# Kernel tuning notes

Hardware: AMD Instinct MI355X
Metric: run time of the kernel (lower is better)

Reference implementation:

```python
import jax, jax.numpy as jnp
import numpy as np
import math

D_MODEL = 1024
NUM_HEADS = 16
HEAD_DIM = D_MODEL // NUM_HEADS
BLOCK_SIZE = 64
THRESHOLD = 0.99


def setup_inputs() -> dict:
    key = jax.random.key(0)
    ks = jax.random.split(key, 12)
    B, S, D = 2, 2048, D_MODEL
    scale = 1.0 / math.sqrt(D)
    x = jax.random.normal(ks[0], (B, S, D), dtype=jnp.float32)
    G_ii = jax.random.uniform(ks[1], (B, S), dtype=jnp.float32)
    # Linear weights stored as [in, out]; applied as x @ W + b (matches nn.Linear math).
    Wq = jax.random.normal(ks[2], (D, D), dtype=jnp.float32) * scale
    bq = jnp.zeros((D,), dtype=jnp.float32)
    Wk = jax.random.normal(ks[3], (D, D), dtype=jnp.float32) * scale
    bk = jnp.zeros((D,), dtype=jnp.float32)
    Wv = jax.random.normal(ks[4], (D, D), dtype=jnp.float32) * scale
    bv = jnp.zeros((D,), dtype=jnp.float32)
    Wo = jax.random.normal(ks[5], (D, D), dtype=jnp.float32) * scale
    bo = jnp.zeros((D,), dtype=jnp.float32)
    return {"x": x, "G_ii": G_ii, "Wq": Wq, "bq": bq, "Wk": Wk, "bk": bk,
            "Wv": Wv, "bv": bv, "Wo": Wo, "bo": bo}


def reference(x, G_ii, Wq, bq, Wk, bk, Wv, bv, Wo, bo):
    B, S, D = x.shape
    H, hd, bs = NUM_HEADS, HEAD_DIM, BLOCK_SIZE
    nb = S // bs

    # Projections and head split: [B, H, S, hd]
    q = (x @ Wq + bq).reshape(B, S, H, hd).transpose(0, 2, 1, 3)
    k = (x @ Wk + bk).reshape(B, S, H, hd).transpose(0, 2, 1, 3)
    v = (x @ Wv + bv).reshape(B, S, H, hd).transpose(0, 2, 1, 3)

    # Per-query-block scattering energy keep mask: block kept iff max |G_ii| >= threshold
    energy = jnp.abs(G_ii)                              # [B, S]
    block_max = energy.reshape(B, nb, bs).max(axis=-1)  # [B, nb]
    keep = (block_max >= THRESHOLD)                     # [B, nb] bool
    row_keep = jnp.repeat(keep, bs, axis=1)             # [B, S]

    # Kept query blocks attend densely (non-causal) over all keys; skipped blocks output zero.
    scores = jnp.einsum('bhqd,bhkd->bhqk', q, k) / math.sqrt(hd)  # [B, H, S, S]
    attn = jax.nn.softmax(scores, axis=-1)
    out = jnp.einsum('bhqk,bhkd->bhqd', attn, v)                  # [B, H, S, hd]
    out = out * row_keep[:, None, :, None].astype(out.dtype)

    out = out.transpose(0, 2, 1, 3).reshape(B, S, D)
    return out @ Wo + bo
```

## Files before the change

kernel.cpp:

```cpp
#include <hip/hip_runtime.h>
#include <math.h>

#define D_MODEL   1024
#define NUM_HEADS 16
#define HEAD_DIM  64
#define BS        64
#define NB        32
#define S_LEN     2048
#define BATCH     2
#define M_ROWS    (BATCH * S_LEN)
#define THRESH    0.99f
#define SCEXP     0.18033688f
#define NPH       (BATCH * NB * NUM_HEADS)

typedef __attribute__((ext_vector_type(8))) short bf16x8;
typedef __attribute__((ext_vector_type(8))) _Float16 f16x8;
typedef __attribute__((ext_vector_type(2))) __fp16 fp16v2;
typedef __attribute__((ext_vector_type(4))) float f32x4;

static constexpr size_t QKV_ELEMS = (size_t)BATCH * NUM_HEADS * S_LEN * HEAD_DIM;

__device__ __forceinline__ unsigned short f2bf(float f) {
    unsigned int u = __float_as_uint(f);
    u += 0x7fff + ((u >> 16) & 1);
    return (unsigned short)(u >> 16);
}

__device__ __forceinline__ unsigned int pkrtz(float a, float b) {
    fp16v2 r = __builtin_amdgcn_cvt_pkrtz(a, b);
    return __builtin_bit_cast(unsigned int, r);
}

__device__ __forceinline__ void gload16(const void* gptr, void* lptr) {
    __builtin_amdgcn_global_load_lds(
        (const __attribute__((address_space(1))) void*)gptr,
        (__attribute__((address_space(3))) void*)lptr, 16, 0, 0);
}

__global__ void compact_kernel(const float* __restrict__ G, int* __restrict__ keep,
                               int* __restrict__ work) {
    int t = threadIdx.x;
    const float4* g = (const float4*)(G + (size_t)t * 64);
    float mx = 0.f;
    #pragma unroll
    for (int i = 0; i < 16; i++) {
        float4 v = g[i];
        mx = fmaxf(mx, fmaxf(fmaxf(fabsf(v.x), fabsf(v.y)), fmaxf(fabsf(v.z), fabsf(v.w))));
    }
    bool k = (mx >= THRESH);
    unsigned long long bal = __ballot(k);
    int nk = __popcll(bal);
    unsigned long long below = bal & ((1ull << t) - 1ull);
    int nbelow = (int)__popcll(below);
    keep[t] = k ? 1 : 0;
    if (t == 0) work[0] = nk;
    int pos = k ? nbelow : (nk + t - nbelow);
    work[1 + pos] = t;
}

__global__ __launch_bounds__(256) void convert_x(const float* __restrict__ x,
                                                 unsigned short* __restrict__ xb) {
    size_t i = ((size_t)blockIdx.x * 256 + threadIdx.x) * 8;
    float4 a = *(const float4*)(x + i);
    float4 b = *(const float4*)(x + i + 4);
    uint4 o;
    o.x = (unsigned int)f2bf(a.x) | ((unsigned int)f2bf(a.y) << 16);
    o.y = (unsigned int)f2bf(a.z) | ((unsigned int)f2bf(a.w) << 16);
    o.z = (unsigned int)f2bf(b.x) | ((unsigned int)f2bf(b.y) << 16);
    o.w = (unsigned int)f2bf(b.z) | ((unsigned int)f2bf(b.w) << 16);
    *(uint4*)(xb + i) = o;
}

__global__ __launch_bounds__(256) void transpose_w(
    const float* __restrict__ Wq, const float* __restrict__ Wk,
    const float* __restrict__ Wv, const float* __restrict__ Wo,
    unsigned short* __restrict__ wcat, unsigned short* __restrict__ wot)
{
    int mat = blockIdx.z;
    const float* W = (mat == 0) ? Wq : (mat == 1) ? Wk : (mat == 2) ? Wv : Wo;
    __shared__ float T[64][65];
    int k0 = blockIdx.x * 64, n0 = blockIdx.y * 64;
    int tid = threadIdx.x;
    int rr = tid >> 4, c4 = (tid & 15) * 4;
    #pragma unroll
    for (int i = 0; i < 4; i++) {
        int row = rr + i * 16;
        float4 v = *(const float4*)(W + (size_t)(k0 + row) * 1024 + n0 + c4);
        T[row][c4 + 0] = v.x; T[row][c4 + 1] = v.y;
        T[row][c4 + 2] = v.z; T[row][c4 + 3] = v.w;
    }
    __syncthreads();
    unsigned short* dst = (mat < 3) ? (wcat + (size_t)mat * 1024 * 1024) : wot;
    #pragma unroll
    for (int i = 0; i < 4; i++) {
        int n = rr + i * 16;
        unsigned int lo = (unsigned int)f2bf(T[c4 + 0][n]) | ((unsigned int)f2bf(T[c4 + 1][n]) << 16);
        unsigned int hi = (unsigned int)f2bf(T[c4 + 2][n]) | ((unsigned int)f2bf(T[c4 + 3][n]) << 16);
        *(uint2*)(dst + (size_t)(n0 + n) * 1024 + k0 + c4) = make_uint2(lo, hi);
    }
}

__global__ __launch_bounds__(256) void mfma_gemm(
    const unsigned short* __restrict__ A, const unsigned short* __restrict__ Bt,
    const float* __restrict__ b0, const float* __restrict__ b1, const float* __restrict__ b2,
    const int* __restrict__ keep,
    void* __restrict__ out0, unsigned short* __restrict__ out1, unsigned short* __restrict__ out2,
    int mode)
{
    const int K = 1024;
    const int n0 = blockIdx.x * 128, m0 = blockIdx.y * 128;
    const int tid = threadIdx.x, w = tid >> 6, lane = tid & 63;
    const int quad = lane >> 4, l16 = lane & 15;
    const int wm = w >> 1, wn = w & 1;

    const int kb0 = m0 >> 6;
    const bool dropped = (!keep[kb0]) && (!keep[kb0 + 1]);

    if (mode == 1 && (n0 >> 10) == 0 && dropped) return;
    if (mode == 0 && dropped) {
        float* o = (float*)out0;
        #pragma unroll
        for (int i = 0; i < 16; i++) {
            int u = tid + i * 256;
            int row = u >> 5, c = (u & 31) * 4;
            *(float4*)(o + (size_t)(m0 + row) * 1024 + n0 + c) = *(const float4*)(b0 + n0 + c);
        }
        return;
    }

    __shared__ unsigned short Asl[2][128 * 32];
    __shared__ unsigned short Bsl[2][128 * 32];

    f32x4 acc[4][4];
    #pragma unroll
    for (int mt = 0; mt < 4; mt++)
        #pragma unroll
        for (int nt = 0; nt < 4; nt++) acc[mt][nt] = (f32x4){0.f, 0.f, 0.f, 0.f};

    #define GSTAGE(it_, p_)                                                             \
        {                                                                               \
            int k0_ = (it_) * 32;                                                       \
            _Pragma("unroll")                                                           \
            for (int j = 0; j < 2; j++) {                                               \
                int s = w * 128 + j * 64 + lane;                                        \
                int row = s >> 2, cl = s & 3;                                           \
                int c = cl ^ ((row >> 1) & 3);                                          \
                gload16(A  + (size_t)(m0 + row) * K + k0_ + c * 8,                      \
                        &Asl[p_][(size_t)(w * 128 + j * 64) * 8]);                      \
                gload16(Bt + (size_t)(n0 + row) * K + k0_ + c * 8,                      \
                        &Bsl[p_][(size_t)(w * 128 + j * 64) * 8]);                      \
            }                                                                           \
        }

    GSTAGE(0, 0)

    for (int it = 0; it < 32; it++) {
        const int p = it & 1;
        __syncthreads();
        if (it + 1 < 32) GSTAGE(it + 1, (it + 1) & 1)

        bf16x8 af[4], bfr[4];
        #pragma unroll
        for (int mt = 0; mt < 4; mt++) {
            int row = wm * 64 + mt * 16 + l16;
            int cl = quad ^ ((row >> 1) & 3);
            af[mt] = *(const bf16x8*)&Asl[p][(row * 4 + cl) * 8];
        }
        #pragma unroll
        for (int nt = 0; nt < 4; nt++) {
            int row = wn * 64 + nt * 16 + l16;
            int cl = quad ^ ((row >> 1) & 3);
            bfr[nt] = *(const bf16x8*)&Bsl[p][(row * 4 + cl) * 8];
        }
        #pragma unroll
        for (int mt = 0; mt < 4; mt++)
            #pragma unroll
            for (int nt = 0; nt < 4; nt++)
                acc[mt][nt] = __builtin_amdgcn_mfma_f32_16x16x32_bf16(af[mt], bfr[nt], acc[mt][nt], 0, 0, 0);
    }

    if (mode == 0) {
        float* o = (float*)out0;
        #pragma unroll
        for (int nt = 0; nt < 4; nt++) {
            int col = n0 + wn * 64 + nt * 16 + l16;
            float bb = b0[col];
            #pragma unroll
            for (int mt = 0; mt < 4; mt++) {
                int mb = m0 + wm * 64 + mt * 16 + quad * 4;
                #pragma unroll
                for (int r = 0; r < 4; r++)
                    o[(size_t)(mb + r) * 1024 + col] = acc[mt][nt][r] + bb;
            }
        }
    } else {
        #pragma unroll
        for (int nt = 0; nt < 4; nt++) {
            int col = n0 + wn * 64 + nt * 16 + l16;
            int kind = col >> 10, cc = col & 1023;
            int h = cc >> 6, d = cc & 63;
            const float* bp = (kind == 0) ? b0 : (kind == 1) ? b1 : b2;
            float bb = bp[cc];
            #pragma unroll
            for (int mt = 0; mt < 4; mt++) {
                int m = m0 + wm * 64 + mt * 16 + quad * 4;
                int b = m >> 11, s = m & 2047;
                if (kind < 2) {
                    unsigned short* dst = ((kind == 0) ? (unsigned short*)out0 : out1) +
                        ((size_t)(b * NUM_HEADS + h) * S_LEN + s) * HEAD_DIM + d;
                    #pragma unroll
                    for (int r = 0; r < 4; r++)
                        dst[(size_t)r * HEAD_DIM] = f2bf(acc[mt][nt][r] + bb);
                } else {
                    unsigned int lo = pkrtz(acc[mt][nt][0] + bb, acc[mt][nt][1] + bb);
                    unsigned int hi = pkrtz(acc[mt][nt][2] + bb, acc[mt][nt][3] + bb);
                    *(uint2*)(out2 + ((size_t)(b * NUM_HEADS + h) * HEAD_DIM + d) * S_LEN + s) =
                        make_uint2(lo, hi);
                }
            }
        }
    }
}

__global__ __launch_bounds__(256, 4) void attn_kernel(
    const unsigned short* __restrict__ Q, const unsigned short* __restrict__ K,
    const unsigned short* __restrict__ Vtg, const int* __restrict__ work,
    unsigned short* __restrict__ opart, float* __restrict__ lpart)
{
    const int bx = blockIdx.x, half = blockIdx.y;
    const int pair = bx >> 4, h = bx & 15;
    const int tid  = threadIdx.x;
    const int w    = tid >> 6, lane = tid & 63;
    const int quad = lane >> 4, l16 = lane & 15;

    if (pair >= work[0]) return;
    const int e = work[1 + pair];
    const int b = e >> 5, qblk = e & 31;

    __shared__ unsigned short Kbuf[2][BS * HEAD_DIM];
    __shared__ unsigned short Vbuf[2][HEAD_DIM * BS];
    __shared__ unsigned short Pt[4][16 * 64];

    const size_t bh = (size_t)(b * NUM_HEADS + h);
    const unsigned short* Kb = K + bh * S_LEN * HEAD_DIM + (size_t)half * 1024 * HEAD_DIM;
    const unsigned short* Vb = Vtg + bh * HEAD_DIM * S_LEN + (size_t)half * 1024;
    const unsigned short* Qb = Q + bh * S_LEN * HEAD_DIM;

    const int qrow = qblk * BS + w * 16 + l16;
    bf16x8 qf[2];
    #pragma unroll
    for (int ks = 0; ks < 2; ks++)
        qf[ks] = *(const bf16x8*)(Qb + (size_t)qrow * HEAD_DIM + ks * 32 + quad * 8);

    f32x4 o[4];
    #pragma unroll
    for (int mt = 0; mt < 4; mt++) o[mt] = (f32x4){0.f, 0.f, 0.f, 0.f};
    float l = 0.f;

    #define STAGE(kc_, p_)                                                              \
        {                                                                               \
            const unsigned short* kg_ = Kb + (size_t)(kc_) * BS * HEAD_DIM;             \
            const unsigned short* vg_ = Vb + (size_t)(kc_) * BS;                        \
            _Pragma("unroll")                                                           \
            for (int j = 0; j < 2; j++) {                                               \
                int s = w * 128 + j * 64 + lane;                                        \
                int row = s >> 3, cs = s & 7;                                           \
                int cg = cs ^ (row & 7);                                                \
                gload16(kg_ + row * 64 + cg * 8,                                        \
                        &Kbuf[p_][(size_t)(w * 128 + j * 64) * 8]);                     \
                gload16(vg_ + (size_t)row * S_LEN + cg * 8,                             \
                        &Vbuf[p_][(size_t)(w * 128 + j * 64) * 8]);                     \
            }                                                                           \
        }

    STAGE(0, 0)

    for (int kc = 0; kc < 16; kc++) {
        const int p = kc & 1;
        __syncthreads();
        if (kc + 1 < 16) STAGE(kc + 1, (kc + 1) & 1)

        const unsigned short* Kp = Kbuf[p];
        const unsigned short* Vp = Vbuf[p];

        f32x4 st[4];
        #pragma unroll
        for (int mt = 0; mt < 4; mt++) {
            f32x4 acc = {0.f, 0.f, 0.f, 0.f};
            #pragma unroll
            for (int ks = 0; ks < 2; ks++) {
                int kk = mt * 16 + l16;
                bf16x8 kf = *(const bf16x8*)&Kp[(size_t)(kk * 8 + ((ks * 4 + quad) ^ (kk & 7))) * 8];
                acc = __builtin_amdgcn_mfma_f32_16x16x32_bf16(kf, qf[ks], acc, 0, 0, 0);
            }
            st[mt] = acc;
        }

        float pv[16], sum = 0.f;
        #pragma unroll
        for (int mt = 0; mt < 4; mt++)
            #pragma unroll
            for (int r = 0; r < 4; r++) {
                float ex = exp2f(st[mt][r] * SCEXP);
                pv[mt * 4 + r] = ex; sum += ex;
            }
        sum += __shfl_xor(sum, 16, 64);
        sum += __shfl_xor(sum, 32, 64);
        l += sum;

        #pragma unroll
        for (int mt = 0; mt < 4; mt++) {
            unsigned int lo = pkrtz(pv[mt * 4 + 0], pv[mt * 4 + 1]);
            unsigned int hi = pkrtz(pv[mt * 4 + 2], pv[mt * 4 + 3]);
            int c16 = 2 * mt + (quad >> 1);
            *(uint2*)&Pt[w][l16 * 64 + ((c16 ^ (l16 & 7)) * 8 + (quad & 1) * 4)] = make_uint2(lo, hi);
        }

        #pragma unroll
        for (int ks = 0; ks < 2; ks++) {
            f16x8 pf = *(const f16x8*)&Pt[w][l16 * 64 + (((4 * ks + quad) ^ (l16 & 7)) * 8)];
            #pragma unroll
            for (int mt = 0; mt < 4; mt++) {
                int d = mt * 16 + l16;
                f16x8 vf = *(const f16x8*)&Vp[(size_t)(d * 8 + ((ks * 4 + quad) ^ (d & 7))) * 8];
                o[mt] = __builtin_amdgcn_mfma_f32_16x16x32_f16(vf, pf, o[mt], 0, 0, 0);
            }
        }
    }

    unsigned short* ob = opart + ((size_t)(half * NPH + bx)) * 4096 + tid * 16;
    uint4 w0, w1;
    w0.x = pkrtz(o[0][0], o[0][1]); w0.y = pkrtz(o[0][2], o[0][3]);
    w0.z = pkrtz(o[1][0], o[1][1]); w0.w = pkrtz(o[1][2], o[1][3]);
    w1.x = pkrtz(o[2][0], o[2][1]); w1.y = pkrtz(o[2][2], o[2][3]);
    w1.z = pkrtz(o[3][0], o[3][1]); w1.w = pkrtz(o[3][2], o[3][3]);
    *(uint4*)ob = w0;
    *(uint4*)(ob + 8) = w1;
    if (quad == 0) lpart[(size_t)(half * NPH + bx) * 64 + w * 16 + l16] = l;
}

__global__ __launch_bounds__(256) void attn_combine(
    const unsigned short* __restrict__ opart, const float* __restrict__ lpart,
    const int* __restrict__ work, unsigned short* __restrict__ attn_out)
{
    const int bx = blockIdx.x;
    const int pair = bx >> 4, h = bx & 15;
    const int tid  = threadIdx.x;
    const int w    = tid >> 6, lane = tid & 63;
    const int quad = lane >> 4, l16 = lane & 15;

    const int e = work[1 + pair];
    const int b = e >> 5, qblk = e & 31;
    unsigned short* ablk = attn_out + ((size_t)(b * S_LEN + qblk * BS)) * D_MODEL + h * HEAD_DIM;

    if (pair >= work[0]) {
        uint4 z = make_uint4(0, 0, 0, 0);
        #pragma unroll
        for (int i = 0; i < 2; i++) {
            int u = tid + i * 256;
            int row = u >> 3, c8 = (u & 7) * 8;
            *(uint4*)(ablk + (size_t)row * D_MODEL + c8) = z;
        }
        return;
    }

    __shared__ float Obuf[4][HEAD_DIM * 17];

    const f16x8* p0 = (const f16x8*)(opart + (size_t)bx * 4096 + tid * 16);
    const f16x8* p1 = (const f16x8*)(opart + ((size_t)NPH + bx) * 4096 + tid * 16);
    f16x8 a0 = p0[0], a1 = p0[1], b0 = p1[0], b1 = p1[1];
    float lsum = lpart[(size_t)bx * 64 + w * 16 + l16] +
                 lpart[((size_t)NPH + bx) * 64 + w * 16 + l16];
    float inv = 1.0f / lsum;

    float osum[16];
    #pragma unroll
    for (int j = 0; j < 8; j++) {
        osum[j]     = (float)a0[j] + (float)b0[j];
        osum[8 + j] = (float)a1[j] + (float)b1[j];
    }
    #pragma unroll
    for (int mt = 0; mt < 4; mt++)
        #pragma unroll
        for (int r = 0; r < 4; r++)
            Obuf[w][(mt * 16 + quad * 4 + r) * 17 + l16] = osum[mt * 4 + r] * inv;
    #pragma unroll
    for (int i = 0; i < 4; i++) {
        int uu = lane + 64 * i;
        int row = uu >> 4, d4 = (uu & 15) * 4;
        float x0 = Obuf[w][(d4 + 0) * 17 + row];
        float x1 = Obuf[w][(d4 + 1) * 17 + row];
        float x2 = Obuf[w][(d4 + 2) * 17 + row];
        float x3 = Obuf[w][(d4 + 3) * 17 + row];
        unsigned int lo = (unsigned int)f2bf(x0) | ((unsigned int)f2bf(x1) << 16);
        unsigned int hi = (unsigned int)f2bf(x2) | ((unsigned int)f2bf(x3) << 16);
        *(uint2*)(ablk + (size_t)(w * 16 + row) * D_MODEL + d4) = make_uint2(lo, hi);
    }
}

extern "C" void kernel_launch(void* const* d_in, const int* in_sizes, int n_in,
                              void* d_out, int out_size, void* d_ws, size_t ws_size,
                              hipStream_t stream) {
    const float* x  = (const float*)d_in[0];
    const float* G  = (const float*)d_in[1];
    const float* Wq = (const float*)d_in[2];
    const float* bq = (const float*)d_in[3];
    const float* Wk = (const float*)d_in[4];
    const float* bk = (const float*)d_in[5];
    const float* Wv = (const float*)d_in[6];
    const float* bv = (const float*)d_in[7];
    const float* Wo = (const float*)d_in[8];
    const float* bo = (const float*)d_in[9];
    float* out = (float*)d_out;

    char* wsp = (char*)d_ws;
    int* keep = (int*)wsp;
    int* work = keep + 64;
    unsigned short* xb    = (unsigned short*)(wsp + 1024);
    unsigned short* wcat  = xb + (size_t)M_ROWS * D_MODEL;
    unsigned short* wot   = wcat + (size_t)3 * 1024 * 1024;
    unsigned short* q     = wot + (size_t)1024 * 1024;
    unsigned short* k     = q + QKV_ELEMS;
    unsigned short* vt    = k + QKV_ELEMS;
    unsigned short* attnb = vt + QKV_ELEMS;
    unsigned short* opart = attnb + (size_t)M_ROWS * D_MODEL;
    float* lpart = (float*)(opart + (size_t)2 * NPH * 4096);

    compact_kernel<<<1, 64, 0, stream>>>(G, keep, work);
    convert_x<<<(M_ROWS * D_MODEL) / (256 * 8), 256, 0, stream>>>(x, xb);
    transpose_w<<<dim3(16, 16, 4), 256, 0, stream>>>(Wq, Wk, Wv, Wo, wcat, wot);

    mfma_gemm<<<dim3(3072 / 128, M_ROWS / 128), 256, 0, stream>>>(
        xb, wcat, bq, bk, bv, keep, (void*)q, k, vt, 1);

    attn_kernel<<<dim3(NPH, 2), 256, 0, stream>>>(q, k, vt, work, opart, lpart);
    attn_combine<<<NPH, 256, 0, stream>>>(opart, lpart, work, attnb);

    mfma_gemm<<<dim3(1024 / 128, M_ROWS / 128), 256, 0, stream>>>(
        attnb, wot, bo, nullptr, nullptr, keep, (void*)out, nullptr, nullptr, 0);
}
```

Baseline: 209.1 us.

## Merge prep kernels into one launch and register-prefetch K/V in attention

Folds the keep-mask compaction, the x bf16 conversion and the weight transposes into a single prep kernel dispatched by block index, cutting two kernel launches. The attention kernel drops its double-buffered LDS staging through global_load_lds and instead prefetches the next K/V tile into registers, then writes it to single-buffered LDS after the compute step. Halving the K/V LDS footprint and raising the launch-bounds occupancy hint from 4 to 6 is meant to fit more resident blocks per CU. In exchange each iteration now needs two barriers and carries more registers for the prefetched tile.

```diff
diff --git a/kernel.cpp b/kernel.cpp
--- a/kernel.cpp
+++ b/kernel.cpp
@@ -37,66 +37,68 @@
         (__attribute__((address_space(3))) void*)lptr, 16, 0, 0);
 }
 
-__global__ void compact_kernel(const float* __restrict__ G, int* __restrict__ keep,
-                               int* __restrict__ work) {
-    int t = threadIdx.x;
-    const float4* g = (const float4*)(G + (size_t)t * 64);
-    float mx = 0.f;
-    #pragma unroll
-    for (int i = 0; i < 16; i++) {
-        float4 v = g[i];
-        mx = fmaxf(mx, fmaxf(fmaxf(fabsf(v.x), fabsf(v.y)), fmaxf(fabsf(v.z), fabsf(v.w))));
-    }
-    bool k = (mx >= THRESH);
-    unsigned long long bal = __ballot(k);
-    int nk = __popcll(bal);
-    unsigned long long below = bal & ((1ull << t) - 1ull);
-    int nbelow = (int)__popcll(below);
-    keep[t] = k ? 1 : 0;
-    if (t == 0) work[0] = nk;
-    int pos = k ? nbelow : (nk + t - nbelow);
-    work[1 + pos] = t;
-}
-
-__global__ __launch_bounds__(256) void convert_x(const float* __restrict__ x,
-                                                 unsigned short* __restrict__ xb) {
-    size_t i = ((size_t)blockIdx.x * 256 + threadIdx.x) * 8;
-    float4 a = *(const float4*)(x + i);
-    float4 b = *(const float4*)(x + i + 4);
-    uint4 o;
-    o.x = (unsigned int)f2bf(a.x) | ((unsigned int)f2bf(a.y) << 16);
-    o.y = (unsigned int)f2bf(a.z) | ((unsigned int)f2bf(a.w) << 16);
-    o.z = (unsigned int)f2bf(b.x) | ((unsigned int)f2bf(b.y) << 16);
-    o.w = (unsigned int)f2bf(b.z) | ((unsigned int)f2bf(b.w) << 16);
-    *(uint4*)(xb + i) = o;
-}
-
-__global__ __launch_bounds__(256) void transpose_w(
+__global__ __launch_bounds__(256) void prep_kernel(
+    const float* __restrict__ x, const float* __restrict__ G,
     const float* __restrict__ Wq, const float* __restrict__ Wk,
     const float* __restrict__ Wv, const float* __restrict__ Wo,
-    unsigned short* __restrict__ wcat, unsigned short* __restrict__ wot)
+    unsigned short* __restrict__ xb, unsigned short* __restrict__ wcat,
+    unsigned short* __restrict__ wot, int* __restrict__ keep, int* __restrict__ work)
 {
-    int mat = blockIdx.z;
-    const float* W = (mat == 0) ? Wq : (mat == 1) ? Wk : (mat == 2) ? Wv : Wo;
+    const int bid = blockIdx.x, tid = threadIdx.x;
     __shared__ float T[64][65];
-    int k0 = blockIdx.x * 64, n0 = blockIdx.y * 64;
-    int tid = threadIdx.x;
-    int rr = tid >> 4, c4 = (tid & 15) * 4;
-    #pragma unroll
-    for (int i = 0; i < 4; i++) {
-        int row = rr + i * 16;
-        float4 v = *(const float4*)(W + (size_t)(k0 + row) * 1024 + n0 + c4);
-        T[row][c4 + 0] = v.x; T[row][c4 + 1] = v.y;
-        T[row][c4 + 2] = v.z; T[row][c4 + 3] = v.w;
-    }
-    __syncthreads();
-    unsigned short* dst = (mat < 3) ? (wcat + (size_t)mat * 1024 * 1024) : wot;
-    #pragma unroll
-    for (int i = 0; i < 4; i++) {
-        int n = rr + i * 16;
-        unsigned int lo = (unsigned int)f2bf(T[c4 + 0][n]) | ((unsigned int)f2bf(T[c4 + 1][n]) << 16);
-        unsigned int hi = (unsigned int)f2bf(T[c4 + 2][n]) | ((unsigned int)f2bf(T[c4 + 3][n]) << 16);
-        *(uint2*)(dst + (size_t)(n0 + n) * 1024 + k0 + c4) = make_uint2(lo, hi);
+
+    if (bid < 2048) {
+        size_t i = ((size_t)bid * 256 + tid) * 8;
+        float4 a = *(const float4*)(x + i);
+        float4 b = *(const float4*)(x + i + 4);
+        uint4 o;
+        o.x = (unsigned int)f2bf(a.x) | ((unsigned int)f2bf(a.y) << 16);
+        o.y = (unsigned int)f2bf(a.z) | ((unsigned int)f2bf(a.w) << 16);
+        o.z = (unsigned int)f2bf(b.x) | ((unsigned int)f2bf(b.y) << 16);
+        o.w = (unsigned int)f2bf(b.z) | ((unsigned int)f2bf(b.w) << 16);
+        *(uint4*)(xb + i) = o;
+    } else if (bid < 3072) {
+        int i = bid - 2048;
+        int mat = i >> 8, rem = i & 255;
+        int k0 = (rem & 15) * 64, n0 = (rem >> 4) * 64;
+        const float* W = (mat == 0) ? Wq : (mat == 1) ? Wk : (mat == 2) ? Wv : Wo;
+        int rr = tid >> 4, c4 = (tid & 15) * 4;
+        #pragma unroll
+        for (int j = 0; j < 4; j++) {
+            int row = rr + j * 16;
+            float4 v = *(const float4*)(W + (size_t)(k0 + row) * 1024 + n0 + c4);
+            T[row][c4 + 0] = v.x; T[row][c4 + 1] = v.y;
+            T[row][c4 + 2] = v.z; T[row][c4 + 3] = v.w;
+        }
+        __syncthreads();
+        unsigned short* dst = (mat < 3) ? (wcat + (size_t)mat * 1024 * 1024) : wot;
+        #pragma unroll
+        for (int j = 0; j < 4; j++) {
+            int n = rr + j * 16;
+            unsigned int lo = (unsigned int)f2bf(T[c4 + 0][n]) | ((unsigned int)f2bf(T[c4 + 1][n]) << 16);
+            unsigned int hi = (unsigned int)f2bf(T[c4 + 2][n]) | ((unsigned int)f2bf(T[c4 + 3][n]) << 16);
+            *(uint2*)(dst + (size_t)(n0 + n) * 1024 + k0 + c4) = make_uint2(lo, hi);
+        }
+    } else {
+        if (tid < 64) {
+            int t = tid;
+            const float4* g = (const float4*)(G + (size_t)t * 64);
+            float mx = 0.f;
+            #pragma unroll
+            for (int j = 0; j < 16; j++) {
+                float4 v = g[j];
+                mx = fmaxf(mx, fmaxf(fmaxf(fabsf(v.x), fabsf(v.y)), fmaxf(fabsf(v.z), fabsf(v.w))));
+            }
+            bool k = (mx >= THRESH);
+            unsigned long long bal = __ballot(k);
+            int nk = __popcll(bal);
+            unsigned long long below = bal & ((1ull << t) - 1ull);
+            int nbelow = (int)__popcll(below);
+            keep[t] = k ? 1 : 0;
+            if (t == 0) work[0] = nk;
+            int pos = k ? nbelow : (nk + t - nbelow);
+            work[1 + pos] = t;
+        }
     }
 }
 
@@ -222,7 +224,7 @@
     }
 }
 
-__global__ __launch_bounds__(256, 4) void attn_kernel(
+__global__ __launch_bounds__(256, 6) void attn_kernel(
     const unsigned short* __restrict__ Q, const unsigned short* __restrict__ K,
     const unsigned short* __restrict__ Vtg, const int* __restrict__ work,
     unsigned short* __restrict__ opart, float* __restrict__ lpart)
@@ -237,8 +239,8 @@
     const int e = work[1 + pair];
     const int b = e >> 5, qblk = e & 31;
 
-    __shared__ unsigned short Kbuf[2][BS * HEAD_DIM];
-    __shared__ unsigned short Vbuf[2][HEAD_DIM * BS];
+    __shared__ unsigned short Kbuf[BS * HEAD_DIM];
+    __shared__ unsigned short Vbuf[HEAD_DIM * BS];
     __shared__ unsigned short Pt[4][16 * 64];
 
     const size_t bh = (size_t)(b * NUM_HEADS + h);
@@ -257,31 +259,34 @@
     for (int mt = 0; mt < 4; mt++) o[mt] = (f32x4){0.f, 0.f, 0.f, 0.f};
     float l = 0.f;
 
-    #define STAGE(kc_, p_)                                                              \
-        {                                                                               \
-            const unsigned short* kg_ = Kb + (size_t)(kc_) * BS * HEAD_DIM;             \
-            const unsigned short* vg_ = Vb + (size_t)(kc_) * BS;                        \
-            _Pragma("unroll")                                                           \
-            for (int j = 0; j < 2; j++) {                                               \
-                int s = w * 128 + j * 64 + lane;                                        \
-                int row = s >> 3, cs = s & 7;                                           \
-                int cg = cs ^ (row & 7);                                                \
-                gload16(kg_ + row * 64 + cg * 8,                                        \
-                        &Kbuf[p_][(size_t)(w * 128 + j * 64) * 8]);                     \
-                gload16(vg_ + (size_t)row * S_LEN + cg * 8,                             \
-                        &Vbuf[p_][(size_t)(w * 128 + j * 64) * 8]);                     \
-            }                                                                           \
-        }
-
-    STAGE(0, 0)
+    const int sA = w * 128 + lane, sB = sA + 64;
+    const int rA = sA >> 3, cA = (sA & 7) ^ (rA & 7);
+    const int rB = sB >> 3, cB = (sB & 7) ^ (rB & 7);
+    const size_t koA = (size_t)rA * HEAD_DIM + cA * 8, koB = (size_t)rB * HEAD_DIM + cB * 8;
+    const size_t voA = (size_t)rA * S_LEN + cA * 8,    voB = (size_t)rB * S_LEN + cB * 8;
+
+    uint4 kr0, kr1, vr0, vr1;
+    #define LOADREGS(kc_)                                                       \
+        {                                                                       \
+            const unsigned short* kg_ = Kb + (size_t)(kc_) * BS * HEAD_DIM;     \
+            const unsigned short* vg_ = Vb + (size_t)(kc_) * BS;                \
+            kr0 = *(const uint4*)(kg_ + koA); kr1 = *(const uint4*)(kg_ + koB); \
+            vr0 = *(const uint4*)(vg_ + voA); vr1 = *(const uint4*)(vg_ + voB); \
+        }
+    #define WRITELDS()                                                          \
+        {                                                                       \
+            *(uint4*)&Kbuf[(size_t)sA * 8] = kr0;                               \
+            *(uint4*)&Kbuf[(size_t)sB * 8] = kr1;                               \
+            *(uint4*)&Vbuf[(size_t)sA * 8] = vr0;                               \
+            *(uint4*)&Vbuf[(size_t)sB * 8] = vr1;                               \
+        }
+
+    LOADREGS(0)
+    WRITELDS()
+    __syncthreads();
 
     for (int kc = 0; kc < 16; kc++) {
-        const int p = kc & 1;
-        __syncthreads();
-        if (kc + 1 < 16) STAGE(kc + 1, (kc + 1) & 1)
-
-        const unsigned short* Kp = Kbuf[p];
-        const unsigned short* Vp = Vbuf[p];
+        if (kc + 1 < 16) LOADREGS(kc + 1)
 
         f32x4 st[4];
         #pragma unroll
@@ -290,7 +295,7 @@
             #pragma unroll
             for (int ks = 0; ks < 2; ks++) {
                 int kk = mt * 16 + l16;
-                bf16x8 kf = *(const bf16x8*)&Kp[(size_t)(kk * 8 + ((ks * 4 + quad) ^ (kk & 7))) * 8];
+                bf16x8 kf = *(const bf16x8*)&Kbuf[(size_t)(kk * 8 + ((ks * 4 + quad) ^ (kk & 7))) * 8];
                 acc = __builtin_amdgcn_mfma_f32_16x16x32_bf16(kf, qf[ks], acc, 0, 0, 0);
             }
             st[mt] = acc;
@@ -322,9 +327,15 @@
             #pragma unroll
             for (int mt = 0; mt < 4; mt++) {
                 int d = mt * 16 + l16;
-                f16x8 vf = *(const f16x8*)&Vp[(size_t)(d * 8 + ((ks * 4 + quad) ^ (d & 7))) * 8];
+                f16x8 vf = *(const f16x8*)&Vbuf[(size_t)(d * 8 + ((ks * 4 + quad) ^ (d & 7))) * 8];
                 o[mt] = __builtin_amdgcn_mfma_f32_16x16x32_f16(vf, pf, o[mt], 0, 0, 0);
             }
+        }
+
+        __syncthreads();
+        if (kc + 1 < 16) {
+            WRITELDS()
+            __syncthreads();
         }
     }
 
@@ -426,9 +437,7 @@
     unsigned short* opart = attnb + (size_t)M_ROWS * D_MODEL;
     float* lpart = (float*)(opart + (size_t)2 * NPH * 4096);
 
-    compact_kernel<<<1, 64, 0, stream>>>(G, keep, work);
-    convert_x<<<(M_ROWS * D_MODEL) / (256 * 8), 256, 0, stream>>>(x, xb);
-    transpose_w<<<dim3(16, 16, 4), 256, 0, stream>>>(Wq, Wk, Wv, Wo, wcat, wot);
+    prep_kernel<<<3073, 256, 0, stream>>>(x, G, Wq, Wk, Wv, Wo, xb, wcat, wot, keep, work);
 
     mfma_gemm<<<dim3(3072 / 128, M_ROWS / 128), 256, 0, stream>>>(
         xb, wcat, bq, bk, bv, keep, (void*)q, k, vt, 1);
```

Result: slower. 227.0 us (+8.6%).
